# Optimization experiments

Measured on AMD Instinct MI355X. Metric: run time of the kernel, lower is better.

The kernel has to match this reference:

```python
import jax, jax.numpy as jnp
import numpy as np
import math

B, Q, K, D = 16, 2048, 2048, 128


def setup_inputs() -> dict:
    key = jax.random.key(0)
    kq, kk, kv, kl = jax.random.split(key, 4)
    queries = jax.random.normal(kq, (B, Q, D), dtype=jnp.float32)
    keys = jax.random.normal(kk, (B, K, D), dtype=jnp.float32)
    values = jax.random.normal(kv, (B, K, D), dtype=jnp.float32)
    valid_lens = jax.random.randint(kl, (B,), 1, K + 1, dtype=jnp.int32)
    return {"queries": queries, "keys": keys, "values": values, "valid_lens": valid_lens}


def reference(queries, keys, values, valid_lens):
    d = queries.shape[-1]
    # scores = bmm(Q, K^T) // sqrt(d)  -- source uses floor-division, kept faithfully
    scores = jnp.floor(jnp.einsum('bqd,bkd->bqk', queries, keys) / math.sqrt(d))
    # masked_softmax: positions >= valid_len[b] get -1e6 before softmax
    mask = jnp.arange(keys.shape[1]) < valid_lens[:, None, None]  # [B,1,K]
    scores = jnp.where(mask, scores, -1e6)
    attn = jax.nn.softmax(scores, axis=-1)
    # dropout in eval mode = identity
    return jnp.einsum('bqk,bkv->bqv', attn, values)
```

## Files before the change

### kernel.cpp

```cpp
#include <hip/hip_runtime.h>
#include <cmath>

typedef __attribute__((ext_vector_type(4))) float f32x4;
typedef __attribute__((ext_vector_type(8))) _Float16 f16x8;
typedef __attribute__((ext_vector_type(4))) _Float16 f16x4;
typedef __attribute__((ext_vector_type(4))) unsigned int u32x4;

#define B_SZ 16
#define Q_SZ 2048
#define K_SZ 2048
#define D_SZ 128
#define BQ   64
#define BKT  64
#define SCL  0.08838834764831845f

#define GLDS16(g, s) __builtin_amdgcn_global_load_lds(                      \
    (const __attribute__((address_space(1))) unsigned int*)(g),             \
    (__attribute__((address_space(3))) unsigned int*)(s), 16, 0, 0)

static __device__ inline unsigned pk16(float a, float b) {
  unsigned short ha = __builtin_bit_cast(unsigned short, (_Float16)a);
  unsigned short hb = __builtin_bit_cast(unsigned short, (_Float16)b);
  return (unsigned)ha | ((unsigned)hb << 16);
}

__global__ __launch_bounds__(256) void prep_all(
    const float* __restrict__ K, const float* __restrict__ V,
    _Float16* __restrict__ Khi, _Float16* __restrict__ Klo,
    _Float16* __restrict__ Vt)
{
  __shared__ _Float16 tmp[64][136];
  const int tid = threadIdx.x;
  if (blockIdx.x < 2048) {
    const int gid = blockIdx.x * 256 + tid;
    const int r = gid >> 4;
    const int g = gid & 15;
    const float* src = K + (size_t)r * D_SZ + g * 8;
    f16x8 hi, lo;
#pragma unroll
    for (int i = 0; i < 8; ++i) {
      float x = src[i];
      _Float16 h = (_Float16)x;
      hi[i] = h;
      lo[i] = (_Float16)((x - (float)h) * 2048.0f);
    }
    const size_t o = (size_t)r * D_SZ + ((g ^ (r & 7)) * 8);
    *(f16x8*)(Khi + o) = hi;
    *(f16x8*)(Klo + o) = lo;
  } else {
    const int vb = blockIdx.x - 2048;
    const int b = vb >> 5;
    const int k0 = (vb & 31) * 64;
    const float* Vb = V + ((size_t)b * K_SZ + k0) * D_SZ;
#pragma unroll
    for (int j = 0; j < 8; ++j) {
      const int e = j * 1024 + tid * 4;
      const int k = e >> 7, d = e & 127;
      const f32x4 v = *(const f32x4*)(Vb + (size_t)k * D_SZ + d);
      f16x4 h;
#pragma unroll
      for (int i = 0; i < 4; ++i) h[i] = (_Float16)v[i];
      *(f16x4*)&tmp[k][d] = h;
    }
    __syncthreads();
#pragma unroll
    for (int i = 0; i < 4; ++i) {
      const int id = i * 256 + tid;
      const int gk = id >> 7, d = id & 127;
      f16x8 o;
#pragma unroll
      for (int jj = 0; jj < 8; ++jj) {
        const int kap = ((gk >> 2) << 5) | ((jj >> 2) << 4) | ((gk & 3) << 2) | (jj & 3);
        o[jj] = tmp[kap][d];
      }
      _Float16* dst = Vt + ((size_t)b * D_SZ + d) * K_SZ + k0 + ((gk ^ (d & 7)) * 8);
      *(f16x8*)dst = o;
    }
  }
}

__global__ __launch_bounds__(256, 3) void attn(
    const float* __restrict__ Qm, const _Float16* __restrict__ KhiG,
    const _Float16* __restrict__ KloG, const _Float16* __restrict__ VtG,
    const int* __restrict__ vlp, float* __restrict__ Om,
    float* __restrict__ P1, float* __restrict__ L0, float* __restrict__ L1,
    unsigned* __restrict__ cnt, const int split)
{
  __shared__ __align__(16) char sm[49152];
  __shared__ float Ls[64];
  __shared__ int s_task;

  const int tid  = threadIdx.x;
  const int wave = tid >> 6;
  const int lane = tid & 63;
  const int ln   = lane & 15;
  const int quad = lane >> 4;

  _Float16* smKhi = (_Float16*)sm;
  _Float16* smKlo = (_Float16*)(sm + 16384);
  _Float16* smVt  = (_Float16*)(sm + 32768);

  for (;;) {
    int t;
    if (split) {
      if (tid == 0) s_task = (int)atomicAdd(cnt, 1u);
      __syncthreads();
      t = s_task;
      __syncthreads();
      if (t >= 1024) return;
    } else {
      t = blockIdx.x;
    }

    int half = 0, b, qt;
    if (split) { half = (t >= 512); const int u = t & 511; b = u >> 5; qt = u & 31; }
    else       { b = t >> 5; qt = t & 31; }
    const int q0     = qt * BQ;
    const int valid  = vlp[b];
    const int kstart = half * 1024;
    const int kend   = split ? min(valid, kstart + 1024) : valid;
    if (kend <= kstart) { if (!split) return; continue; }
    const int ntiles = (kend - kstart + BKT - 1) / BKT;

    const float* Qb    = Qm + (size_t)b * Q_SZ * D_SZ;
    const char*  gKhiB = (const char*)KhiG + (size_t)b * K_SZ * 256;
    const char*  gKloB = (const char*)KloG + (size_t)b * K_SZ * 256;
    const char*  gVtB  = (const char*)VtG  + (size_t)b * D_SZ * (K_SZ * 2);

    f16x8 qhi[4], qlo[4];
    {
      const int qrow = q0 + wave * 16 + ln;
      const float* srcb = Qb + (size_t)qrow * D_SZ + quad * 8;
#pragma unroll
      for (int c = 0; c < 4; ++c) {
#pragma unroll
        for (int j = 0; j < 8; ++j) {
          float x = srcb[c * 32 + j];
          _Float16 h = (_Float16)x;
          qhi[c][j] = h;
          qlo[c][j] = (_Float16)((x - (float)h) * 2048.0f);
        }
      }
    }

    const f32x4 vzero = {0.f, 0.f, 0.f, 0.f};
    f32x4 accO[8];
    float lsum = 0.0f;
#pragma unroll
    for (int dt = 0; dt < 8; ++dt) accO[dt] = vzero;

    for (int kt = 0; kt < ntiles; ++kt) {
      const int k0g = kstart + kt * BKT;

      if (kt) {
        asm volatile("s_waitcnt lgkmcnt(0)" ::: "memory");
        __builtin_amdgcn_sched_barrier(0);
        __builtin_amdgcn_s_barrier();
        __builtin_amdgcn_sched_barrier(0);
      }

      {
        const char* gh = gKhiB + (size_t)k0g * 256;
        const char* gl = gKloB + (size_t)k0g * 256;
#pragma unroll
        for (int i = 0; i < 4; ++i) {
          const int off = wave * 1024 + i * 4096;
          GLDS16(gh + off + lane * 16, sm + off);
        }
#pragma unroll
        for (int i = 0; i < 4; ++i) {
          const int off = wave * 1024 + i * 4096;
          GLDS16(gl + off + lane * 16, sm + 16384 + off);
        }
#pragma unroll
        for (int i = 0; i < 4; ++i) {
          const int off = wave * 1024 + i * 4096;
          const int a = off + lane * 16;
          const int d = a >> 7, win = a & 127;
          GLDS16(gVtB + (size_t)d * (K_SZ * 2) + (size_t)k0g * 2 + win,
                 sm + 32768 + off);
        }
      }
      asm volatile("s_waitcnt vmcnt(0)" ::: "memory");
      __builtin_amdgcn_sched_barrier(0);
      __builtin_amdgcn_s_barrier();
      __builtin_amdgcn_sched_barrier(0);

      f16x8 pa[2];
#pragma unroll
      for (int hk = 0; hk < 2; ++hk) {
        f32x4 accM[2], accC[2];
#pragma unroll
        for (int nb2 = 0; nb2 < 2; ++nb2) { accM[nb2] = vzero; accC[nb2] = vzero; }
        __builtin_amdgcn_s_setprio(1);
#pragma unroll
        for (int nb2 = 0; nb2 < 2; ++nb2) {
          const int row = (hk * 2 + nb2) * 16 + ln;
          const _Float16* bh_base = smKhi + row * 128;
          const _Float16* bl_base = smKlo + row * 128;
#pragma unroll
          for (int c = 0; c < 4; ++c) {
            const int pg = (((c * 4 + quad) ^ (ln & 7)) * 8);
            const f16x8 bh = *(const f16x8*)(bh_base + pg);
            const f16x8 bl = *(const f16x8*)(bl_base + pg);
            accM[nb2] = __builtin_amdgcn_mfma_f32_16x16x32_f16(bh, qhi[c], accM[nb2], 0, 0, 0);
            accC[nb2] = __builtin_amdgcn_mfma_f32_16x16x32_f16(bl, qhi[c], accC[nb2], 0, 0, 0);
            accC[nb2] = __builtin_amdgcn_mfma_f32_16x16x32_f16(bh, qlo[c], accC[nb2], 0, 0, 0);
          }
        }
        __builtin_amdgcn_s_setprio(0);

        u32x4 w;
#pragma unroll
        for (int nb2 = 0; nb2 < 2; ++nb2) {
          float e[4];
#pragma unroll
          for (int r = 0; r < 4; ++r) {
            const int key = k0g + (hk * 2 + nb2) * 16 + quad * 4 + r;
            const float s = accM[nb2][r] + accC[nb2][r] * (1.0f / 2048.0f);
            e[r] = (key < valid) ? __expf(floorf(s * SCL)) : 0.0f;
            lsum += e[r];
          }
          w[nb2 * 2 + 0] = pk16(e[0], e[1]);
          w[nb2 * 2 + 1] = pk16(e[2], e[3]);
        }
        pa[hk] = __builtin_bit_cast(f16x8, w);
      }

      __builtin_amdgcn_s_setprio(1);
#pragma unroll
      for (int c = 0; c < 2; ++c) {
#pragma unroll
        for (int dt = 0; dt < 8; ++dt) {
          const int drow = dt * 16 + ln;
          const int pg = (((c * 4 + quad) ^ (ln & 7)) * 8);
          const f16x8 bf = *(const f16x8*)(smVt + drow * 64 + pg);
          accO[dt] = __builtin_amdgcn_mfma_f32_16x16x32_f16(pa[c], bf, accO[dt], 0, 0, 0);
        }
      }
      __builtin_amdgcn_s_setprio(0);
    }

    {
      float v = lsum;
      v += __shfl_xor(v, 16, 64);
      v += __shfl_xor(v, 32, 64);
      lsum = v;
    }

    if (split) {
      float* Lh = half ? L1 : L0;
      if (lane < 16)
        atomicAdd(Lh + b * Q_SZ + q0 + wave * 16 + lane, lsum);
      float* dst = (half ? P1 : Om) + ((size_t)(b * Q_SZ + q0)) * D_SZ;
#pragma unroll
      for (int dt = 0; dt < 8; ++dt)
#pragma unroll
        for (int r = 0; r < 4; ++r)
          dst[(size_t)(wave * 16 + quad * 4 + r) * D_SZ + dt * 16 + ln] =
              accO[dt][r];
    } else {
      if (lane < 16) Ls[wave * 16 + lane] = lsum;
      __syncthreads();
      float* Ob = Om + (size_t)b * Q_SZ * D_SZ;
#pragma unroll
      for (int r = 0; r < 4; ++r) {
        const float inv = 1.0f / Ls[wave * 16 + quad * 4 + r];
#pragma unroll
        for (int dt = 0; dt < 8; ++dt)
          Ob[(size_t)(q0 + wave * 16 + quad * 4 + r) * D_SZ + dt * 16 + ln] =
              accO[dt][r] * inv;
      }
    }
    if (!split) return;
  }
}

__global__ __launch_bounds__(256) void finalize(
    float* __restrict__ Om, const float* __restrict__ P1,
    const float* __restrict__ L0, const float* __restrict__ L1,
    const int* __restrict__ vlp)
{
  const int idx = blockIdx.x * 256 + threadIdx.x;
  const size_t e = (size_t)idx * 4;
  const int row = (int)(e >> 7);
  const int b = row >> 11;
  const int valid = vlp[b];
  f32x4 o = *(const f32x4*)(Om + e);
  float l = L0[row];
  if (valid > 1024) {
    const f32x4 p = *(const f32x4*)(P1 + e);
    o += p;
    l += L1[row];
  }
  const float inv = 1.0f / l;
  o *= inv;
  *(f32x4*)(Om + e) = o;
}

extern "C" void kernel_launch(void* const* d_in, const int* in_sizes, int n_in,
                              void* d_out, int out_size, void* d_ws, size_t ws_size,
                              hipStream_t stream) {
  const float* Qm = (const float*)d_in[0];
  const float* Km = (const float*)d_in[1];
  const float* Vm = (const float*)d_in[2];
  const int*   vl = (const int*)d_in[3];
  float*       Om = (float*)d_out;

  const size_t elems = (size_t)B_SZ * K_SZ * D_SZ;
  const size_t PREP  = 3 * elems * sizeof(_Float16);
  const size_t HDR   = 262400;
  const size_t P1SZ  = elems * sizeof(float);
  char* W = (char*)d_ws;

  if (ws_size >= HDR + PREP + P1SZ) {
    unsigned* cnt = (unsigned*)W;
    float*    L0  = (float*)(W + 256);
    float*    L1  = (float*)(W + 256 + 131072);
    _Float16* Khi = (_Float16*)(W + HDR);
    _Float16* Klo = Khi + elems;
    _Float16* Vt  = Klo + elems;
    float*    P1  = (float*)(W + HDR + PREP);
    hipMemsetAsync(d_ws, 0, HDR, stream);
    prep_all<<<2560, 256, 0, stream>>>(Km, Vm, Khi, Klo, Vt);
    attn<<<768, 256, 0, stream>>>(Qm, Khi, Klo, Vt, vl, Om, P1, L0, L1, cnt, 1);
    finalize<<<4096, 256, 0, stream>>>(Om, P1, L0, L1, vl);
  } else {
    _Float16* Khi = (_Float16*)W;
    _Float16* Klo = Khi + elems;
    _Float16* Vt  = Klo + elems;
    prep_all<<<2560, 256, 0, stream>>>(Km, Vm, Khi, Klo, Vt);
    attn<<<512, 256, 0, stream>>>(Qm, Khi, Klo, Vt, vl, Om,
                                  nullptr, nullptr, nullptr, nullptr, 0);
  }
}
```

Baseline: 164.7 us.

## Prefetch next K/V tile into registers while computing current tile

Replaces the direct global-to-LDS loads, which were waited on before each tile's compute, with register staging. The next tile is loaded into registers at the start of each iteration, overlapping global latency with the MFMA work, then written to LDS after a barrier. This adds 48 VGPRs of staging per thread, an extra barrier per tile, and explicit LDS store instructions, which may reduce occupancy.

```diff
diff --git a/kernel.cpp b/kernel.cpp
--- a/kernel.cpp
+++ b/kernel.cpp
@@ -13,10 +13,6 @@
 #define BQ   64
 #define BKT  64
 #define SCL  0.08838834764831845f
-
-#define GLDS16(g, s) __builtin_amdgcn_global_load_lds(                      \
-    (const __attribute__((address_space(1))) unsigned int*)(g),             \
-    (__attribute__((address_space(3))) unsigned int*)(s), 16, 0, 0)
 
 static __device__ inline unsigned pk16(float a, float b) {
   unsigned short ha = __builtin_bit_cast(unsigned short, (_Float16)a);
@@ -127,6 +123,36 @@
     const char*  gKloB = (const char*)KloG + (size_t)b * K_SZ * 256;
     const char*  gVtB  = (const char*)VtG  + (size_t)b * D_SZ * (K_SZ * 2);
 
+    f32x4 stg[12];
+    auto LOADSTG = [&](int k0g) {
+      const char* gh = gKhiB + (size_t)k0g * 256;
+      const char* gl = gKloB + (size_t)k0g * 256;
+#pragma unroll
+      for (int i = 0; i < 4; ++i)
+        stg[i] = *(const f32x4*)(gh + wave * 1024 + i * 4096 + lane * 16);
+#pragma unroll
+      for (int i = 0; i < 4; ++i)
+        stg[4 + i] = *(const f32x4*)(gl + wave * 1024 + i * 4096 + lane * 16);
+#pragma unroll
+      for (int i = 0; i < 4; ++i) {
+        const int off = wave * 1024 + i * 4096;
+        const int a = off + lane * 16;
+        const int d = a >> 7, win = a & 127;
+        stg[8 + i] = *(const f32x4*)(gVtB + (size_t)d * (K_SZ * 2) + (size_t)k0g * 2 + win);
+      }
+    };
+    auto WRITESTG = [&]() {
+#pragma unroll
+      for (int i = 0; i < 4; ++i)
+        *(f32x4*)(sm + wave * 1024 + i * 4096 + lane * 16) = stg[i];
+#pragma unroll
+      for (int i = 0; i < 4; ++i)
+        *(f32x4*)(sm + 16384 + wave * 1024 + i * 4096 + lane * 16) = stg[4 + i];
+#pragma unroll
+      for (int i = 0; i < 4; ++i)
+        *(f32x4*)(sm + 32768 + wave * 1024 + i * 4096 + lane * 16) = stg[8 + i];
+    };
+
     f16x8 qhi[4], qlo[4];
     {
       const int qrow = q0 + wave * 16 + ln;
@@ -149,41 +175,18 @@
 #pragma unroll
     for (int dt = 0; dt < 8; ++dt) accO[dt] = vzero;
 
+    LOADSTG(kstart);
+    WRITESTG();
+    asm volatile("s_waitcnt lgkmcnt(0)" ::: "memory");
+    __builtin_amdgcn_sched_barrier(0);
+    __builtin_amdgcn_s_barrier();
+    __builtin_amdgcn_sched_barrier(0);
+
     for (int kt = 0; kt < ntiles; ++kt) {
       const int k0g = kstart + kt * BKT;
-
-      if (kt) {
-        asm volatile("s_waitcnt lgkmcnt(0)" ::: "memory");
-        __builtin_amdgcn_sched_barrier(0);
-        __builtin_amdgcn_s_barrier();
-        __builtin_amdgcn_sched_barrier(0);
-      }
-
-      {
-        const char* gh = gKhiB + (size_t)k0g * 256;
-        const char* gl = gKloB + (size_t)k0g * 256;
-#pragma unroll
-        for (int i = 0; i < 4; ++i) {
-          const int off = wave * 1024 + i * 4096;
-          GLDS16(gh + off + lane * 16, sm + off);
-        }
-#pragma unroll
-        for (int i = 0; i < 4; ++i) {
-          const int off = wave * 1024 + i * 4096;
-          GLDS16(gl + off + lane * 16, sm + 16384 + off);
-        }
-#pragma unroll
-        for (int i = 0; i < 4; ++i) {
-          const int off = wave * 1024 + i * 4096;
-          const int a = off + lane * 16;
-          const int d = a >> 7, win = a & 127;
-          GLDS16(gVtB + (size_t)d * (K_SZ * 2) + (size_t)k0g * 2 + win,
-                 sm + 32768 + off);
-        }
-      }
-      asm volatile("s_waitcnt vmcnt(0)" ::: "memory");
-      __builtin_amdgcn_sched_barrier(0);
-      __builtin_amdgcn_s_barrier();
+      const bool more = (kt + 1 < ntiles);
+
+      if (more) LOADSTG(k0g + BKT);
       __builtin_amdgcn_sched_barrier(0);
 
       f16x8 pa[2];
@@ -239,6 +242,18 @@
         }
       }
       __builtin_amdgcn_s_setprio(0);
+
+      asm volatile("s_waitcnt lgkmcnt(0)" ::: "memory");
+      __builtin_amdgcn_sched_barrier(0);
+      __builtin_amdgcn_s_barrier();
+      __builtin_amdgcn_sched_barrier(0);
+      if (more) {
+        WRITESTG();
+        asm volatile("s_waitcnt lgkmcnt(0)" ::: "memory");
+        __builtin_amdgcn_sched_barrier(0);
+        __builtin_amdgcn_s_barrier();
+        __builtin_amdgcn_sched_barrier(0);
+      }
     }
 
     {
```

Measured after the change: 183.0 us. 1.11x slower.

## Fuse split-K merge into attention kernel and schedule longest tasks first

Applied to the files above, without the earlier changes.

Removes the separate finalize kernel. Batches whose valid length fits in one half now normalize and write output directly. For two-half batches, the last block to finish (tracked by a per-tile atomic counter) merges both partials. Tasks are also reordered so the halves with the most key tiles are dequeued first, which should improve load balance, and the memset shrinks to just the counters. In exchange it adds threadfences, extra barriers and a tail merge inside the attention kernel.

```diff
diff --git a/kernel.cpp b/kernel.cpp
--- a/kernel.cpp
+++ b/kernel.cpp
@@ -84,11 +84,14 @@
     const _Float16* __restrict__ KloG, const _Float16* __restrict__ VtG,
     const int* __restrict__ vlp, float* __restrict__ Om,
     float* __restrict__ P1, float* __restrict__ L0, float* __restrict__ L1,
-    unsigned* __restrict__ cnt, const int split)
+    unsigned* __restrict__ done, unsigned* __restrict__ cnt, const int split)
 {
   __shared__ __align__(16) char sm[49152];
   __shared__ float Ls[64];
   __shared__ int s_task;
+  __shared__ unsigned s_old;
+  __shared__ signed char ord[32];
+  __shared__ int vls[16];
 
   const int tid  = threadIdx.x;
   const int wave = tid >> 6;
@@ -99,6 +102,27 @@
   _Float16* smKhi = (_Float16*)sm;
   _Float16* smKlo = (_Float16*)(sm + 16384);
   _Float16* smVt  = (_Float16*)(sm + 32768);
+
+  if (split) {
+    if (tid < 16) vls[tid] = vlp[tid];
+    __syncthreads();
+    if (tid < 32) {
+      const int ub = tid >> 1, uh = tid & 1;
+      const int v = vls[ub];
+      const int n = uh ? ((v > 1024) ? (v - 1024 + 63) / 64 : 0)
+                       : (((v < 1024 ? v : 1024) + 63) / 64);
+      int rank = 0;
+      for (int u = 0; u < 32; ++u) {
+        const int wb = u >> 1, wh = u & 1;
+        const int wv = vls[wb];
+        const int wn = wh ? ((wv > 1024) ? (wv - 1024 + 63) / 64 : 0)
+                          : (((wv < 1024 ? wv : 1024) + 63) / 64);
+        rank += (wn > n) || (wn == n && u < tid);
+      }
+      ord[rank] = (signed char)tid;
+    }
+    __syncthreads();
+  }
 
   for (;;) {
     int t;
@@ -113,10 +137,10 @@
     }
 
     int half = 0, b, qt;
-    if (split) { half = (t >= 512); const int u = t & 511; b = u >> 5; qt = u & 31; }
+    if (split) { const int u = ord[t >> 5]; b = u >> 1; half = u & 1; qt = t & 31; }
     else       { b = t >> 5; qt = t & 31; }
     const int q0     = qt * BQ;
-    const int valid  = vlp[b];
+    const int valid  = split ? vls[b] : vlp[b];
     const int kstart = half * 1024;
     const int kend   = split ? min(valid, kstart + 1024) : valid;
     if (kend <= kstart) { if (!split) return; continue; }
@@ -249,16 +273,54 @@
     }
 
     if (split) {
-      float* Lh = half ? L1 : L0;
-      if (lane < 16)
-        atomicAdd(Lh + b * Q_SZ + q0 + wave * 16 + lane, lsum);
-      float* dst = (half ? P1 : Om) + ((size_t)(b * Q_SZ + q0)) * D_SZ;
-#pragma unroll
-      for (int dt = 0; dt < 8; ++dt)
-#pragma unroll
-        for (int r = 0; r < 4; ++r)
-          dst[(size_t)(wave * 16 + quad * 4 + r) * D_SZ + dt * 16 + ln] =
-              accO[dt][r];
+      const bool two = (valid > 1024);
+      if (!two) {
+        if (lane < 16) Ls[wave * 16 + lane] = lsum;
+        __syncthreads();
+        float* Ob = Om + (size_t)b * Q_SZ * D_SZ;
+#pragma unroll
+        for (int r = 0; r < 4; ++r) {
+          const float inv = 1.0f / Ls[wave * 16 + quad * 4 + r];
+#pragma unroll
+          for (int dt = 0; dt < 8; ++dt)
+            Ob[(size_t)(q0 + wave * 16 + quad * 4 + r) * D_SZ + dt * 16 + ln] =
+                accO[dt][r] * inv;
+        }
+        __syncthreads();
+      } else {
+        float* Lh = half ? L1 : L0;
+        if (lane < 16)
+          Lh[b * Q_SZ + q0 + wave * 16 + lane] = lsum;
+        float* dst = (half ? P1 : Om) + ((size_t)(b * Q_SZ + q0)) * D_SZ;
+#pragma unroll
+        for (int dt = 0; dt < 8; ++dt)
+#pragma unroll
+          for (int r = 0; r < 4; ++r)
+            dst[(size_t)(wave * 16 + quad * 4 + r) * D_SZ + dt * 16 + ln] =
+                accO[dt][r];
+        __threadfence();
+        __syncthreads();
+        if (tid == 0) s_old = atomicAdd(done + (b * 32 + qt), 1u);
+        __syncthreads();
+        if (s_old == 1) {
+          __threadfence();
+          const size_t base = (size_t)(b * Q_SZ + q0) * D_SZ;
+          const int lrow = b * Q_SZ + q0;
+#pragma unroll
+          for (int i = 0; i < 8; ++i) {
+            const int idx = i * 256 + tid;
+            const int r = idx >> 5;
+            const size_t e = base + (size_t)idx * 4;
+            f32x4 o = *(const f32x4*)(Om + e);
+            const f32x4 p = *(const f32x4*)(P1 + e);
+            o += p;
+            const float l = L0[lrow + r] + L1[lrow + r];
+            const float inv = 1.0f / l;
+            o *= inv;
+            *(f32x4*)(Om + e) = o;
+          }
+        }
+      }
     } else {
       if (lane < 16) Ls[wave * 16 + lane] = lsum;
       __syncthreads();
@@ -274,28 +336,6 @@
     }
     if (!split) return;
   }
-}
-
-__global__ __launch_bounds__(256) void finalize(
-    float* __restrict__ Om, const float* __restrict__ P1,
-    const float* __restrict__ L0, const float* __restrict__ L1,
-    const int* __restrict__ vlp)
-{
-  const int idx = blockIdx.x * 256 + threadIdx.x;
-  const size_t e = (size_t)idx * 4;
-  const int row = (int)(e >> 7);
-  const int b = row >> 11;
-  const int valid = vlp[b];
-  f32x4 o = *(const f32x4*)(Om + e);
-  float l = L0[row];
-  if (valid > 1024) {
-    const f32x4 p = *(const f32x4*)(P1 + e);
-    o += p;
-    l += L1[row];
-  }
-  const float inv = 1.0f / l;
-  o *= inv;
-  *(f32x4*)(Om + e) = o;
 }
 
 extern "C" void kernel_launch(void* const* d_in, const int* in_sizes, int n_in,
@@ -309,28 +349,28 @@
 
   const size_t elems = (size_t)B_SZ * K_SZ * D_SZ;
   const size_t PREP  = 3 * elems * sizeof(_Float16);
-  const size_t HDR   = 262400;
+  const size_t HDR   = 266240;
   const size_t P1SZ  = elems * sizeof(float);
   char* W = (char*)d_ws;
 
   if (ws_size >= HDR + PREP + P1SZ) {
-    unsigned* cnt = (unsigned*)W;
-    float*    L0  = (float*)(W + 256);
-    float*    L1  = (float*)(W + 256 + 131072);
-    _Float16* Khi = (_Float16*)(W + HDR);
-    _Float16* Klo = Khi + elems;
-    _Float16* Vt  = Klo + elems;
-    float*    P1  = (float*)(W + HDR + PREP);
-    hipMemsetAsync(d_ws, 0, HDR, stream);
+    unsigned* cnt  = (unsigned*)W;
+    unsigned* done = (unsigned*)(W + 256);
+    float*    L0   = (float*)(W + 4096);
+    float*    L1   = (float*)(W + 135168);
+    _Float16* Khi  = (_Float16*)(W + HDR);
+    _Float16* Klo  = Khi + elems;
+    _Float16* Vt   = Klo + elems;
+    float*    P1   = (float*)(W + HDR + PREP);
+    hipMemsetAsync(d_ws, 0, 2304, stream);
     prep_all<<<2560, 256, 0, stream>>>(Km, Vm, Khi, Klo, Vt);
-    attn<<<768, 256, 0, stream>>>(Qm, Khi, Klo, Vt, vl, Om, P1, L0, L1, cnt, 1);
-    finalize<<<4096, 256, 0, stream>>>(Om, P1, L0, L1, vl);
+    attn<<<768, 256, 0, stream>>>(Qm, Khi, Klo, Vt, vl, Om, P1, L0, L1, done, cnt, 1);
   } else {
     _Float16* Khi = (_Float16*)W;
     _Float16* Klo = Khi + elems;
     _Float16* Vt  = Klo + elems;
     prep_all<<<2560, 256, 0, stream>>>(Km, Vm, Khi, Klo, Vt);
     attn<<<512, 256, 0, stream>>>(Qm, Khi, Klo, Vt, vl, Om,
-                                  nullptr, nullptr, nullptr, nullptr, 0);
+                                  nullptr, nullptr, nullptr, nullptr, nullptr, 0);
   }
 }
```

New measurement: 275.5 us. 67.2% more time.

## Order split attention tasks longest-first and drop workspace memset

Applied to the files above, without the earlier changes.

Each attention block now computes the key-tile count for every (batch, half) work unit from valid_lens and ranks the units in descending order. The atomic task counter is then mapped through that ranking, so the longest units are handed out first, which is meant to shorten the tail of the persistent schedule. The separate hipMemsetAsync launch is removed: the prep kernel resets the counter, and the per-row softmax sums are written with plain stores instead of atomicAdd. The catch is that L1 is no longer zeroed for batches whose keys fit in the first half, so correctness depends on finalize not reading it in that case.

```diff
diff --git a/kernel.cpp b/kernel.cpp
--- a/kernel.cpp
+++ b/kernel.cpp
@@ -27,10 +27,11 @@
 __global__ __launch_bounds__(256) void prep_all(
     const float* __restrict__ K, const float* __restrict__ V,
     _Float16* __restrict__ Khi, _Float16* __restrict__ Klo,
-    _Float16* __restrict__ Vt)
+    _Float16* __restrict__ Vt, unsigned* __restrict__ cnt)
 {
   __shared__ _Float16 tmp[64][136];
   const int tid = threadIdx.x;
+  if (cnt && blockIdx.x == 0 && tid == 0) *cnt = 0;
   if (blockIdx.x < 2048) {
     const int gid = blockIdx.x * 256 + tid;
     const int r = gid >> 4;
@@ -89,6 +90,8 @@
   __shared__ __align__(16) char sm[49152];
   __shared__ float Ls[64];
   __shared__ int s_task;
+  __shared__ signed char ord[32];
+  __shared__ int vls[16];
 
   const int tid  = threadIdx.x;
   const int wave = tid >> 6;
@@ -99,6 +102,27 @@
   _Float16* smKhi = (_Float16*)sm;
   _Float16* smKlo = (_Float16*)(sm + 16384);
   _Float16* smVt  = (_Float16*)(sm + 32768);
+
+  if (split) {
+    if (tid < 16) vls[tid] = vlp[tid];
+    __syncthreads();
+    if (tid < 32) {
+      const int ub = tid >> 1, uh = tid & 1;
+      const int v = vls[ub];
+      const int n = uh ? ((v > 1024) ? (v - 1024 + 63) / 64 : 0)
+                       : (((v < 1024 ? v : 1024) + 63) / 64);
+      int rank = 0;
+      for (int u = 0; u < 32; ++u) {
+        const int wb = u >> 1, wh = u & 1;
+        const int wv = vls[wb];
+        const int wn = wh ? ((wv > 1024) ? (wv - 1024 + 63) / 64 : 0)
+                          : (((wv < 1024 ? wv : 1024) + 63) / 64);
+        rank += (wn > n) || (wn == n && u < tid);
+      }
+      ord[rank] = (signed char)tid;
+    }
+    __syncthreads();
+  }
 
   for (;;) {
     int t;
@@ -113,10 +137,10 @@
     }
 
     int half = 0, b, qt;
-    if (split) { half = (t >= 512); const int u = t & 511; b = u >> 5; qt = u & 31; }
+    if (split) { const int u = ord[t >> 5]; b = u >> 1; half = u & 1; qt = t & 31; }
     else       { b = t >> 5; qt = t & 31; }
     const int q0     = qt * BQ;
-    const int valid  = vlp[b];
+    const int valid  = split ? vls[b] : vlp[b];
     const int kstart = half * 1024;
     const int kend   = split ? min(valid, kstart + 1024) : valid;
     if (kend <= kstart) { if (!split) return; continue; }
@@ -251,7 +275,7 @@
     if (split) {
       float* Lh = half ? L1 : L0;
       if (lane < 16)
-        atomicAdd(Lh + b * Q_SZ + q0 + wave * 16 + lane, lsum);
+        Lh[b * Q_SZ + q0 + wave * 16 + lane] = lsum;
       float* dst = (half ? P1 : Om) + ((size_t)(b * Q_SZ + q0)) * D_SZ;
 #pragma unroll
       for (int dt = 0; dt < 8; ++dt)
@@ -321,15 +345,14 @@
     _Float16* Klo = Khi + elems;
     _Float16* Vt  = Klo + elems;
     float*    P1  = (float*)(W + HDR + PREP);
-    hipMemsetAsync(d_ws, 0, HDR, stream);
-    prep_all<<<2560, 256, 0, stream>>>(Km, Vm, Khi, Klo, Vt);
+    prep_all<<<2560, 256, 0, stream>>>(Km, Vm, Khi, Klo, Vt, cnt);
     attn<<<768, 256, 0, stream>>>(Qm, Khi, Klo, Vt, vl, Om, P1, L0, L1, cnt, 1);
     finalize<<<4096, 256, 0, stream>>>(Om, P1, L0, L1, vl);
   } else {
     _Float16* Khi = (_Float16*)W;
     _Float16* Klo = Khi + elems;
     _Float16* Vt  = Klo + elems;
-    prep_all<<<2560, 256, 0, stream>>>(Km, Vm, Khi, Klo, Vt);
+    prep_all<<<2560, 256, 0, stream>>>(Km, Vm, Khi, Klo, Vt, nullptr);
     attn<<<512, 256, 0, stream>>>(Qm, Khi, Klo, Vt, vl, Om,
                                   nullptr, nullptr, nullptr, nullptr, 0);
   }
```

New measurement: 160.6 us. -2.5%, faster.
